# Performance work log

Measured on AMD Instinct MI355X. Metric: run time of the kernel, lower is better.

Reference implementation:

```python
import jax, jax.numpy as jnp
import numpy as np

N_NODES = 50000
N_EDGES = 1600000
NFEAT = 512
HIDDEN = 128
NUM_CLASSES = 40
DROPOUT = 0.5


def setup_inputs() -> dict:
    key = jax.random.key(0)
    ks = jax.random.split(key, 8)
    x = jax.random.normal(ks[0], (N_NODES, NFEAT), dtype=jnp.float32)
    edge_row = jax.random.randint(ks[1], (N_EDGES,), 0, N_NODES, dtype=jnp.int32)
    edge_col = jax.random.randint(ks[2], (N_EDGES,), 0, N_NODES, dtype=jnp.int32)
    edge_vals = jax.random.uniform(ks[3], (N_EDGES,), dtype=jnp.float32)
    # uniform(-stdv, stdv) init as in reset_parameters
    stdv1 = 1.0 / np.sqrt(HIDDEN)
    stdv2 = 1.0 / np.sqrt(NUM_CLASSES)
    W1 = jax.random.uniform(ks[4], (NFEAT, HIDDEN), dtype=jnp.float32, minval=-stdv1, maxval=stdv1)
    b1 = jax.random.uniform(ks[5], (HIDDEN,), dtype=jnp.float32, minval=-stdv1, maxval=stdv1)
    W2 = jax.random.uniform(ks[6], (HIDDEN, NUM_CLASSES), dtype=jnp.float32, minval=-stdv2, maxval=stdv2)
    b2 = jax.random.uniform(ks[7], (NUM_CLASSES,), dtype=jnp.float32, minval=-stdv2, maxval=stdv2)
    return {"x": x, "edge_row": edge_row, "edge_col": edge_col, "edge_vals": edge_vals,
            "W1": W1, "b1": b1, "W2": W2, "b2": b2}


def _spmm(edge_row, edge_col, edge_vals, support):
    # out[i] = sum_{e: row[e]==i} vals[e] * support[col[e]]  (sparse adj @ support)
    msgs = support[edge_col] * edge_vals[:, None]  # [E, F]
    return jax.ops.segment_sum(msgs, edge_row, num_segments=N_NODES)


def _dropout(x, rate, key):
    keep = 1.0 - rate
    mask = jax.random.bernoulli(key, keep, x.shape)
    return jnp.where(mask, x / keep, jnp.zeros((), x.dtype))


def reference(x, edge_row, edge_col, edge_vals, W1, b1, W2, b2):
    # layer 1: GCN conv + bias + relu + dropout (training=True)
    h = _spmm(edge_row, edge_col, edge_vals, x @ W1) + b1  # [N, H]
    h = jax.nn.relu(h)
    h = _dropout(h, DROPOUT, jax.random.key(42))
    # layer 2: GCN conv + bias + relu
    out = _spmm(edge_row, edge_col, edge_vals, h @ W2) + b2  # [N, C]
    return jax.nn.relu(out)
```

## Files before the change

kernel.cpp:

```cpp
#include <hip/hip_runtime.h>
#include <hip/hip_bf16.h>

#define N_NODES 50000
#define N_EDGES 1600000
#define NFEAT   512
#define HIDDEN  128
#define NCLASS  40

#define NBUCK 391
#define ROWS_PER_BUCKET 128
#define BUCK_PAD 4608

#define W1T_BLOCKS 256
#define GEMM1_BLOCKS 391
#define PART_T 4096
#define PART_BLOCKS 391

#define FUSED_LDS 37944

typedef short short8 __attribute__((ext_vector_type(8)));
typedef float f32x4  __attribute__((ext_vector_type(4)));

__device__ __forceinline__ unsigned short f2bu(float f) {
  __hip_bfloat16 h = __float2bfloat16(f);
  return *reinterpret_cast<unsigned short*>(&h);
}

__device__ __forceinline__ unsigned rotl32(unsigned x, int n) {
  return (x << n) | (x >> (32 - n));
}

__device__ __forceinline__ unsigned threefry_bits(unsigned x1) {
  unsigned x0 = 0u;
  const unsigned ks0 = 0u, ks1 = 42u, ks2 = 0x1BD11BDAu ^ 42u;
  x0 += ks0; x1 += ks1;
#define TFR(r) { x0 += x1; x1 = rotl32(x1, (r)); x1 ^= x0; }
  TFR(13) TFR(15) TFR(26) TFR(6)
  x0 += ks1; x1 += ks2 + 1u;
  TFR(17) TFR(29) TFR(16) TFR(24)
  x0 += ks2; x1 += ks0 + 2u;
  TFR(13) TFR(15) TFR(26) TFR(6)
  x0 += ks0; x1 += ks1 + 3u;
  TFR(17) TFR(29) TFR(16) TFR(24)
  x0 += ks1; x1 += ks2 + 4u;
  TFR(13) TFR(15) TFR(26) TFR(6)
  x0 += ks2; x1 += ks0 + 5u;
#undef TFR
  return x0 ^ x1;
}

__global__ __launch_bounds__(256) void init_w1t_kernel(
    const float* __restrict__ W1, unsigned short* __restrict__ W1T,
    int* __restrict__ gcur) {
  if (blockIdx.x < W1T_BLOCKS) {
    int id = blockIdx.x * 256 + threadIdx.x;
    int n = id & 127, k = id >> 7;
    W1T[n * NFEAT + k] = f2bu(W1[k * HIDDEN + n]);
  } else {
    int b = threadIdx.x;
    if (b < NBUCK) gcur[b] = b * BUCK_PAD;
    b += 256;
    if (b < NBUCK) gcur[b] = b * BUCK_PAD;
  }
}

__device__ __forceinline__ void gemm1_body(
    int bid, char* smem, const float* __restrict__ x,
    const unsigned short* __restrict__ W1T,
    unsigned short* __restrict__ support) {
  short8* As = (short8*)smem;
  short8* Bs = (short8*)(smem + 8192);
  const int t = threadIdx.x;
  const int lane = t & 63;
  const int w = t >> 6;
  const int quad = lane >> 4;
  const int l15 = lane & 15;
  const int node_base = bid * 128;
  const int mbase = (w >> 1) * 64;
  const int nbase = (w & 1) * 64;

  f32x4 acc[4][4] = {};

  for (int k0 = 0; k0 < NFEAT; k0 += 32) {
#pragma unroll
    for (int i = 0; i < 2; i++) {
      int lin = i * 256 + t;
      int n = lin >> 2, q = lin & 3;
      int row = node_base + n;
      if (row >= N_NODES) row = N_NODES - 1;
      const float* src = &x[(size_t)row * NFEAT + k0 + q * 8];
      float4 a = *(const float4*)src;
      float4 b = *(const float4*)(src + 4);
      short8 p;
      p[0] = (short)f2bu(a.x); p[1] = (short)f2bu(a.y);
      p[2] = (short)f2bu(a.z); p[3] = (short)f2bu(a.w);
      p[4] = (short)f2bu(b.x); p[5] = (short)f2bu(b.y);
      p[6] = (short)f2bu(b.z); p[7] = (short)f2bu(b.w);
      As[q * 128 + n] = p;
      Bs[q * 128 + n] = *(const short8*)&W1T[(size_t)n * NFEAT + k0 + q * 8];
    }
    __syncthreads();
    short8 af[4], bfr[4];
#pragma unroll
    for (int mt = 0; mt < 4; mt++)
      af[mt] = As[quad * 128 + mbase + mt * 16 + l15];
#pragma unroll
    for (int nt = 0; nt < 4; nt++)
      bfr[nt] = Bs[quad * 128 + nbase + nt * 16 + l15];
#pragma unroll
    for (int mt = 0; mt < 4; mt++)
#pragma unroll
      for (int nt = 0; nt < 4; nt++)
        acc[mt][nt] = __builtin_amdgcn_mfma_f32_16x16x32_bf16(
            af[mt], bfr[nt], acc[mt][nt], 0, 0, 0);
    __syncthreads();
  }

#pragma unroll
  for (int mt = 0; mt < 4; mt++)
#pragma unroll
    for (int nt = 0; nt < 4; nt++)
#pragma unroll
      for (int r = 0; r < 4; r++) {
        int row = node_base + mbase + mt * 16 + quad * 4 + r;
        int col = nbase + nt * 16 + l15;
        if (row < N_NODES)
          support[(size_t)row * HIDDEN + col] = f2bu(acc[mt][nt][r]);
      }
}

__device__ __forceinline__ void partition_body(
    int bid, char* smem, const int* __restrict__ erow,
    const int* __restrict__ ecol, const float* __restrict__ evals,
    int* __restrict__ gcur, uint2* __restrict__ eb) {
  uint2* sorted = (uint2*)smem;
  int* cnt   = (int*)(smem + 32768);
  int* shift = (int*)(smem + 32768 + 1564);
  int* ssc   = (int*)(smem + 32768 + 3128);
  const int t = threadIdx.x;
  const int base = bid * PART_T;

  if (t < NBUCK) cnt[t] = 0;
  if (t + 256 < NBUCK) cnt[t + 256] = 0;
  __syncthreads();

  uint2 er[16];
  unsigned short loc[16];
#pragma unroll
  for (int k = 0; k < 16; k++) {
    int idx = base + k * 256 + t;
    if (idx < N_EDGES) {
      int r = erow[idx];
      er[k].y = (unsigned)r;
      er[k].x = (unsigned)ecol[idx] | ((unsigned)f2bu(evals[idx]) << 16);
      loc[k] = (unsigned short)atomicAdd(&cnt[r >> 7], 1);
    } else {
      er[k].y = 0xffffffffu;
    }
  }
  __syncthreads();

  ssc[t] = (t < NBUCK) ? cnt[t] : 0;
  ssc[t + 256] = (t + 256 < NBUCK) ? cnt[t + 256] : 0;
  __syncthreads();
#pragma unroll
  for (int off = 1; off < 512; off <<= 1) {
    int v0 = (t >= off) ? ssc[t - off] : 0;
    int v1 = ssc[t + 256 - off];
    __syncthreads();
    ssc[t] += v0; ssc[t + 256] += v1;
    __syncthreads();
  }

  for (int b = t; b < NBUCK; b += 256) {
    int c = cnt[b];
    if (c > 0) {
      int lb = ssc[b] - c;
      int gb = atomicAdd(&gcur[b], c);
      shift[b] = gb - lb;
    }
  }
#pragma unroll
  for (int k = 0; k < 16; k++) {
    if (er[k].y != 0xffffffffu) {
      int b = (int)(er[k].y >> 7);
      sorted[ssc[b] - cnt[b] + (int)loc[k]] = er[k];
    }
  }
  __syncthreads();

  const int total = ssc[NBUCK - 1];
  for (int i = t; i < total; i += 256) {
    uint2 e = sorted[i];
    eb[shift[e.y >> 7] + i] = e;
  }
}

__global__ __launch_bounds__(256) void part_gemm1_kernel(
    const int* __restrict__ erow, const int* __restrict__ ecol,
    const float* __restrict__ evals, int* __restrict__ gcur,
    uint2* __restrict__ eb, const float* __restrict__ x,
    const unsigned short* __restrict__ W1T,
    unsigned short* __restrict__ support) {
  __shared__ char smem[FUSED_LDS];
  if (blockIdx.x < PART_BLOCKS)
    partition_body(blockIdx.x, smem, erow, ecol, evals, gcur, eb);
  else
    gemm1_body(blockIdx.x - PART_BLOCKS, smem, x, W1T, support);
}

__global__ __launch_bounds__(512) void csr_build_kernel(
    const uint2* __restrict__ eb, const int* __restrict__ gcur,
    unsigned* __restrict__ csr, int* __restrict__ rowptr,
    int* __restrict__ rowend) {
  __shared__ int cnt[ROWS_PER_BUCKET];
  __shared__ int sc[ROWS_PER_BUCKET];
  __shared__ int cur[ROWS_PER_BUCKET];
  const int t = threadIdx.x;
  const int b = blockIdx.x;
  if (t < ROWS_PER_BUCKET) cnt[t] = 0;
  __syncthreads();
  const int beg = b * BUCK_PAD;
  const int end = gcur[b];
  for (int j = beg + t; j < end; j += 512)
    atomicAdd(&cnt[eb[j].y & 127u], 1);
  __syncthreads();
  if (t < ROWS_PER_BUCKET) sc[t] = cnt[t];
  __syncthreads();
#pragma unroll
  for (int off = 1; off < ROWS_PER_BUCKET; off <<= 1) {
    int v = 0;
    if (t >= off && t < ROWS_PER_BUCKET) v = sc[t - off];
    __syncthreads();
    if (t < ROWS_PER_BUCKET) sc[t] += v;
    __syncthreads();
  }
  if (t < ROWS_PER_BUCKET) {
    int excl = sc[t] - cnt[t];
    cur[t] = excl;
    int row = b * ROWS_PER_BUCKET + t;
    if (row < N_NODES) {
      rowptr[row] = beg + excl;
      rowend[row] = beg + sc[t];
    }
  }
  __syncthreads();
  for (int j = beg + t; j < end; j += 512) {
    uint2 e = eb[j];
    int p = atomicAdd(&cur[e.y & 127u], 1);
    csr[beg + p] = e.x;
  }
}

__global__ __launch_bounds__(256) void spmm1_fused(
    const unsigned* __restrict__ csr, const int* __restrict__ rowptr,
    const int* __restrict__ rowend,
    const unsigned* __restrict__ sup,
    const float* __restrict__ b1, const float* __restrict__ W2,
    unsigned* __restrict__ h2u) {
  __shared__ float Ws[HIDDEN * NCLASS];
  __shared__ unsigned hrow[4][64];
  const int t = threadIdx.x;
#pragma unroll
  for (int i = 0; i < 20; i++) Ws[i * 256 + t] = W2[i * 256 + t];
  __syncthreads();

  const int row = blockIdx.x * 4 + (t >> 6);
  const int wv = t >> 6;
  const int lane = t & 63;
  const int beg = __builtin_amdgcn_readfirstlane(rowptr[row]);
  const int end = __builtin_amdgcn_readfirstlane(rowend[row]);
  float ax = 0.f, ay = 0.f;
  int j = beg;
  for (; j + 15 < end; j += 16) {
    unsigned ps[16];
#pragma unroll
    for (int k = 0; k < 16; k++)
      ps[k] = __builtin_amdgcn_readfirstlane(csr[j + k]);
    unsigned u[16];
#pragma unroll
    for (int k = 0; k < 16; k++)
      u[k] = sup[(size_t)(ps[k] & 0xffffu) * 64 + lane];
#pragma unroll
    for (int k = 0; k < 16; k++) {
      float v = __uint_as_float(ps[k] & 0xffff0000u);
      ax += v * __uint_as_float(u[k] << 16);
      ay += v * __uint_as_float(u[k] & 0xffff0000u);
    }
  }
  for (; j + 7 < end; j += 8) {
    unsigned ps[8];
#pragma unroll
    for (int k = 0; k < 8; k++)
      ps[k] = __builtin_amdgcn_readfirstlane(csr[j + k]);
    unsigned u[8];
#pragma unroll
    for (int k = 0; k < 8; k++)
      u[k] = sup[(size_t)(ps[k] & 0xffffu) * 64 + lane];
#pragma unroll
    for (int k = 0; k < 8; k++) {
      float v = __uint_as_float(ps[k] & 0xffff0000u);
      ax += v * __uint_as_float(u[k] << 16);
      ay += v * __uint_as_float(u[k] & 0xffff0000u);
    }
  }
  for (; j + 1 < end; j += 2) {
    unsigned p0 = __builtin_amdgcn_readfirstlane(csr[j]);
    unsigned p1 = __builtin_amdgcn_readfirstlane(csr[j + 1]);
    unsigned u0 = sup[(size_t)(p0 & 0xffffu) * 64 + lane];
    unsigned u1 = sup[(size_t)(p1 & 0xffffu) * 64 + lane];
    float v0 = __uint_as_float(p0 & 0xffff0000u);
    float v1 = __uint_as_float(p1 & 0xffff0000u);
    ax += v0 * __uint_as_float(u0 << 16) + v1 * __uint_as_float(u1 << 16);
    ay += v0 * __uint_as_float(u0 & 0xffff0000u) +
          v1 * __uint_as_float(u1 & 0xffff0000u);
  }
  if (j < end) {
    unsigned p0 = __builtin_amdgcn_readfirstlane(csr[j]);
    unsigned u0 = sup[(size_t)(p0 & 0xffffu) * 64 + lane];
    float v0 = __uint_as_float(p0 & 0xffff0000u);
    ax += v0 * __uint_as_float(u0 << 16);
    ay += v0 * __uint_as_float(u0 & 0xffff0000u);
  }
  const unsigned i0 = (unsigned)row * HIDDEN + lane * 2;
  float vx = fmaxf(ax + b1[lane * 2], 0.f);
  float vy = fmaxf(ay + b1[lane * 2 + 1], 0.f);
  vx = (threefry_bits(i0) >> 31) ? 0.f : 2.f * vx;
  vy = (threefry_bits(i0 + 1) >> 31) ? 0.f : 2.f * vy;
  hrow[wv][lane] = (unsigned)f2bu(vx) | ((unsigned)f2bu(vy) << 16);
  __syncthreads();

  float accv = 0.f;
  if (lane < NCLASS) {
#pragma unroll 8
    for (int i = 0; i < 64; i++) {
      unsigned u = hrow[wv][i];
      float h0 = __uint_as_float(u << 16);
      float h1 = __uint_as_float(u & 0xffff0000u);
      accv += h0 * Ws[(2 * i) * NCLASS + lane] +
              h1 * Ws[(2 * i + 1) * NCLASS + lane];
    }
    float other = __shfl_xor(accv, 1);
    if (!(lane & 1))
      h2u[(unsigned)row * 20 + (lane >> 1)] =
          (unsigned)f2bu(accv) | ((unsigned)f2bu(other) << 16);
  }
}

__global__ __launch_bounds__(256) void spmm2_fused(
    const unsigned* __restrict__ csr, const int* __restrict__ rowptr,
    const int* __restrict__ rowend,
    const unsigned* __restrict__ h2u,
    const float* __restrict__ b2, float* __restrict__ out) {
  const int row = blockIdx.x * 4 + (threadIdx.x >> 6);
  const int lane = threadIdx.x & 63;
  const int half = lane >> 5;
  const int il = lane & 31;
  const unsigned ilc = (il < 20) ? (unsigned)il : 19u;
  const int beg = rowptr[row], end = rowend[row];
  float ax = 0.f, ay = 0.f;
  int j = beg + half;
  for (; j + 6 < end; j += 8) {
    unsigned p[4], u[4];
#pragma unroll
    for (int k = 0; k < 4; k++) p[k] = csr[j + 2 * k];
#pragma unroll
    for (int k = 0; k < 4; k++) u[k] = h2u[(p[k] & 0xffffu) * 20 + ilc];
#pragma unroll
    for (int k = 0; k < 4; k++) {
      float v = __uint_as_float(p[k] & 0xffff0000u);
      ax += v * __uint_as_float(u[k] << 16);
      ay += v * __uint_as_float(u[k] & 0xffff0000u);
    }
  }
  for (; j + 2 < end; j += 4) {
    unsigned p0 = csr[j];
    unsigned p1 = csr[j + 2];
    unsigned u0 = h2u[(p0 & 0xffffu) * 20 + ilc];
    unsigned u1 = h2u[(p1 & 0xffffu) * 20 + ilc];
    float v0 = __uint_as_float(p0 & 0xffff0000u);
    float v1 = __uint_as_float(p1 & 0xffff0000u);
    ax += v0 * __uint_as_float(u0 << 16) + v1 * __uint_as_float(u1 << 16);
    ay += v0 * __uint_as_float(u0 & 0xffff0000u) +
          v1 * __uint_as_float(u1 & 0xffff0000u);
  }
  for (; j < end; j += 2) {
    unsigned p0 = csr[j];
    unsigned u0 = h2u[(p0 & 0xffffu) * 20 + ilc];
    float v0 = __uint_as_float(p0 & 0xffff0000u);
    ax += v0 * __uint_as_float(u0 << 16);
    ay += v0 * __uint_as_float(u0 & 0xffff0000u);
  }
  ax += __shfl_xor(ax, 32);
  ay += __shfl_xor(ay, 32);
  if (half == 0 && il < 20) {
    float2 r;
    r.x = fmaxf(ax + b2[il * 2], 0.f);
    r.y = fmaxf(ay + b2[il * 2 + 1], 0.f);
    *(float2*)&out[(unsigned)row * NCLASS + il * 2] = r;
  }
}

extern "C" void kernel_launch(void* const* d_in, const int* in_sizes, int n_in,
                              void* d_out, int out_size, void* d_ws,
                              size_t ws_size, hipStream_t stream) {
  const float* x     = (const float*)d_in[0];
  const int*   erow  = (const int*)d_in[1];
  const int*   ecol  = (const int*)d_in[2];
  const float* evals = (const float*)d_in[3];
  const float* W1    = (const float*)d_in[4];
  const float* b1    = (const float*)d_in[5];
  const float* W2    = (const float*)d_in[6];
  const float* b2    = (const float*)d_in[7];
  float* out = (float*)d_out;

  char* base = (char*)d_ws;
  unsigned short* support = (unsigned short*)base;
  uint2*          eb  = (uint2*)(base + 12800000);
  unsigned*       h2  = (unsigned*)(base + 27213824);
  unsigned short* W1T = (unsigned short*)(base + 31213824);
  unsigned*       csr = (unsigned*)(base + 31344896);
  int* rowptr = (int*)(base + 38551808);
  int* rowend = (int*)(base + 38751808);
  int* gcur   = (int*)(base + 38951808);

  init_w1t_kernel<<<W1T_BLOCKS + 1, 256, 0, stream>>>(W1, W1T, gcur);
  part_gemm1_kernel<<<PART_BLOCKS + GEMM1_BLOCKS, 256, 0, stream>>>(
      erow, ecol, evals, gcur, eb, x, W1T, support);
  csr_build_kernel<<<NBUCK, 512, 0, stream>>>(eb, gcur, csr, rowptr, rowend);
  spmm1_fused<<<N_NODES / 4, 256, 0, stream>>>(
      csr, rowptr, rowend, (const unsigned*)support, b1, W2, h2);
  spmm2_fused<<<N_NODES / 4, 256, 0, stream>>>(csr, rowptr, rowend,
                                               (const unsigned*)h2, b2, out);
}
```

Measured before the change: 313.3 us.

## Store support in fp32, use fp32 hidden row, and restructure partition into two-pass bucketing

The GEMM1 output (support) is now stored as fp32 rather than bf16, and spmm1 gathers float2 per lane while keeping the post-dropout hidden row in fp32 for the W2 product. The edge partition step now handles 8192 edges per block and runs two passes: it counts first, then scatters using atomic cursors, so it no longer holds edges in registers. These changes improve accuracy and alter partition occupancy, but they double the bytes gathered in spmm1 and double the LDS per block.

Result: slower. 346.5 us (+10.6%).

```diff
diff --git a/kernel.cpp b/kernel.cpp
--- a/kernel.cpp
+++ b/kernel.cpp
@@ -13,10 +13,10 @@
 
 #define W1T_BLOCKS 256
 #define GEMM1_BLOCKS 391
-#define PART_T 4096
-#define PART_BLOCKS 391
-
-#define FUSED_LDS 37944
+#define PART_T 8192
+#define PART_BLOCKS 196
+
+#define FUSED_LDS 72276
 
 typedef short short8 __attribute__((ext_vector_type(8)));
 typedef float f32x4  __attribute__((ext_vector_type(4)));
@@ -67,7 +67,7 @@
 __device__ __forceinline__ void gemm1_body(
     int bid, char* smem, const float* __restrict__ x,
     const unsigned short* __restrict__ W1T,
-    unsigned short* __restrict__ support) {
+    float* __restrict__ support) {
   short8* As = (short8*)smem;
   short8* Bs = (short8*)(smem + 8192);
   const int t = threadIdx.x;
@@ -125,7 +125,7 @@
         int row = node_base + mbase + mt * 16 + quad * 4 + r;
         int col = nbase + nt * 16 + l15;
         if (row < N_NODES)
-          support[(size_t)row * HIDDEN + col] = f2bu(acc[mt][nt][r]);
+          support[(size_t)row * HIDDEN + col] = acc[mt][nt][r];
       }
 }
 
@@ -134,9 +134,10 @@
     const int* __restrict__ ecol, const float* __restrict__ evals,
     int* __restrict__ gcur, uint2* __restrict__ eb) {
   uint2* sorted = (uint2*)smem;
-  int* cnt   = (int*)(smem + 32768);
-  int* shift = (int*)(smem + 32768 + 1564);
-  int* ssc   = (int*)(smem + 32768 + 3128);
+  int* cnt   = (int*)(smem + 65536);
+  int* cur   = (int*)(smem + 65536 + 1564);
+  int* shift = (int*)(smem + 65536 + 3128);
+  int* ssc   = (int*)(smem + 65536 + 4692);
   const int t = threadIdx.x;
   const int base = bid * PART_T;
 
@@ -144,47 +145,42 @@
   if (t + 256 < NBUCK) cnt[t + 256] = 0;
   __syncthreads();
 
-  uint2 er[16];
-  unsigned short loc[16];
-#pragma unroll
-  for (int k = 0; k < 16; k++) {
+#pragma unroll 8
+  for (int k = 0; k < 32; k++) {
+    int idx = base + k * 256 + t;
+    if (idx < N_EDGES) atomicAdd(&cnt[erow[idx] >> 7], 1);
+  }
+  __syncthreads();
+
+  ssc[t] = (t < NBUCK) ? cnt[t] : 0;
+  ssc[t + 256] = (t + 256 < NBUCK) ? cnt[t + 256] : 0;
+  __syncthreads();
+#pragma unroll
+  for (int off = 1; off < 512; off <<= 1) {
+    int v0 = (t >= off) ? ssc[t - off] : 0;
+    int v1 = ssc[t + 256 - off];
+    __syncthreads();
+    ssc[t] += v0; ssc[t + 256] += v1;
+    __syncthreads();
+  }
+
+  for (int b = t; b < NBUCK; b += 256) {
+    int c = cnt[b];
+    int lb = ssc[b] - c;
+    cur[b] = lb;
+    if (c > 0) shift[b] = atomicAdd(&gcur[b], c) - lb;
+  }
+  __syncthreads();
+
+#pragma unroll 8
+  for (int k = 0; k < 32; k++) {
     int idx = base + k * 256 + t;
     if (idx < N_EDGES) {
       int r = erow[idx];
-      er[k].y = (unsigned)r;
-      er[k].x = (unsigned)ecol[idx] | ((unsigned)f2bu(evals[idx]) << 16);
-      loc[k] = (unsigned short)atomicAdd(&cnt[r >> 7], 1);
-    } else {
-      er[k].y = 0xffffffffu;
-    }
-  }
-  __syncthreads();
-
-  ssc[t] = (t < NBUCK) ? cnt[t] : 0;
-  ssc[t + 256] = (t + 256 < NBUCK) ? cnt[t + 256] : 0;
-  __syncthreads();
-#pragma unroll
-  for (int off = 1; off < 512; off <<= 1) {
-    int v0 = (t >= off) ? ssc[t - off] : 0;
-    int v1 = ssc[t + 256 - off];
-    __syncthreads();
-    ssc[t] += v0; ssc[t + 256] += v1;
-    __syncthreads();
-  }
-
-  for (int b = t; b < NBUCK; b += 256) {
-    int c = cnt[b];
-    if (c > 0) {
-      int lb = ssc[b] - c;
-      int gb = atomicAdd(&gcur[b], c);
-      shift[b] = gb - lb;
-    }
-  }
-#pragma unroll
-  for (int k = 0; k < 16; k++) {
-    if (er[k].y != 0xffffffffu) {
-      int b = (int)(er[k].y >> 7);
-      sorted[ssc[b] - cnt[b] + (int)loc[k]] = er[k];
+      unsigned rec = (unsigned)ecol[idx] | ((unsigned)f2bu(evals[idx]) << 16);
+      int p = atomicAdd(&cur[r >> 7], 1);
+      uint2 e; e.x = rec; e.y = (unsigned)r;
+      sorted[p] = e;
     }
   }
   __syncthreads();
@@ -201,7 +197,7 @@
     const float* __restrict__ evals, int* __restrict__ gcur,
     uint2* __restrict__ eb, const float* __restrict__ x,
     const unsigned short* __restrict__ W1T,
-    unsigned short* __restrict__ support) {
+    float* __restrict__ support) {
   __shared__ char smem[FUSED_LDS];
   if (blockIdx.x < PART_BLOCKS)
     partition_body(blockIdx.x, smem, erow, ecol, evals, gcur, eb);
@@ -255,11 +251,11 @@
 __global__ __launch_bounds__(256) void spmm1_fused(
     const unsigned* __restrict__ csr, const int* __restrict__ rowptr,
     const int* __restrict__ rowend,
-    const unsigned* __restrict__ sup,
+    const float2* __restrict__ sup,
     const float* __restrict__ b1, const float* __restrict__ W2,
     unsigned* __restrict__ h2u) {
   __shared__ float Ws[HIDDEN * NCLASS];
-  __shared__ unsigned hrow[4][64];
+  __shared__ float hrowf[4][HIDDEN];
   const int t = threadIdx.x;
 #pragma unroll
   for (int i = 0; i < 20; i++) Ws[i * 256 + t] = W2[i * 256 + t];
@@ -277,15 +273,15 @@
 #pragma unroll
     for (int k = 0; k < 16; k++)
       ps[k] = __builtin_amdgcn_readfirstlane(csr[j + k]);
-    unsigned u[16];
+    float2 u[16];
 #pragma unroll
     for (int k = 0; k < 16; k++)
       u[k] = sup[(size_t)(ps[k] & 0xffffu) * 64 + lane];
 #pragma unroll
     for (int k = 0; k < 16; k++) {
       float v = __uint_as_float(ps[k] & 0xffff0000u);
-      ax += v * __uint_as_float(u[k] << 16);
-      ay += v * __uint_as_float(u[k] & 0xffff0000u);
+      ax += v * u[k].x;
+      ay += v * u[k].y;
     }
   }
   for (; j + 7 < end; j += 8) {
@@ -293,53 +289,48 @@
 #pragma unroll
     for (int k = 0; k < 8; k++)
       ps[k] = __builtin_amdgcn_readfirstlane(csr[j + k]);
-    unsigned u[8];
+    float2 u[8];
 #pragma unroll
     for (int k = 0; k < 8; k++)
       u[k] = sup[(size_t)(ps[k] & 0xffffu) * 64 + lane];
 #pragma unroll
     for (int k = 0; k < 8; k++) {
       float v = __uint_as_float(ps[k] & 0xffff0000u);
-      ax += v * __uint_as_float(u[k] << 16);
-      ay += v * __uint_as_float(u[k] & 0xffff0000u);
+      ax += v * u[k].x;
+      ay += v * u[k].y;
     }
   }
   for (; j + 1 < end; j += 2) {
     unsigned p0 = __builtin_amdgcn_readfirstlane(csr[j]);
     unsigned p1 = __builtin_amdgcn_readfirstlane(csr[j + 1]);
-    unsigned u0 = sup[(size_t)(p0 & 0xffffu) * 64 + lane];
-    unsigned u1 = sup[(size_t)(p1 & 0xffffu) * 64 + lane];
+    float2 u0 = sup[(size_t)(p0 & 0xffffu) * 64 + lane];
+    float2 u1 = sup[(size_t)(p1 & 0xffffu) * 64 + lane];
     float v0 = __uint_as_float(p0 & 0xffff0000u);
     float v1 = __uint_as_float(p1 & 0xffff0000u);
-    ax += v0 * __uint_as_float(u0 << 16) + v1 * __uint_as_float(u1 << 16);
-    ay += v0 * __uint_as_float(u0 & 0xffff0000u) +
-          v1 * __uint_as_float(u1 & 0xffff0000u);
+    ax += v0 * u0.x + v1 * u1.x;
+    ay += v0 * u0.y + v1 * u1.y;
   }
   if (j < end) {
     unsigned p0 = __builtin_amdgcn_readfirstlane(csr[j]);
-    unsigned u0 = sup[(size_t)(p0 & 0xffffu) * 64 + lane];
+    float2 u0 = sup[(size_t)(p0 & 0xffffu) * 64 + lane];
     float v0 = __uint_as_float(p0 & 0xffff0000u);
-    ax += v0 * __uint_as_float(u0 << 16);
-    ay += v0 * __uint_as_float(u0 & 0xffff0000u);
+    ax += v0 * u0.x;
+    ay += v0 * u0.y;
   }
   const unsigned i0 = (unsigned)row * HIDDEN + lane * 2;
   float vx = fmaxf(ax + b1[lane * 2], 0.f);
   float vy = fmaxf(ay + b1[lane * 2 + 1], 0.f);
   vx = (threefry_bits(i0) >> 31) ? 0.f : 2.f * vx;
   vy = (threefry_bits(i0 + 1) >> 31) ? 0.f : 2.f * vy;
-  hrow[wv][lane] = (unsigned)f2bu(vx) | ((unsigned)f2bu(vy) << 16);
+  hrowf[wv][lane * 2] = vx;
+  hrowf[wv][lane * 2 + 1] = vy;
   __syncthreads();
 
   float accv = 0.f;
   if (lane < NCLASS) {
-#pragma unroll 8
-    for (int i = 0; i < 64; i++) {
-      unsigned u = hrow[wv][i];
-      float h0 = __uint_as_float(u << 16);
-      float h1 = __uint_as_float(u & 0xffff0000u);
-      accv += h0 * Ws[(2 * i) * NCLASS + lane] +
-              h1 * Ws[(2 * i + 1) * NCLASS + lane];
-    }
+#pragma unroll
+    for (int i = 0; i < HIDDEN; i++)
+      accv += hrowf[wv][i] * Ws[i * NCLASS + lane];
     float other = __shfl_xor(accv, 1);
     if (!(lane & 1))
       h2u[(unsigned)row * 20 + (lane >> 1)] =
@@ -415,21 +406,21 @@
   float* out = (float*)d_out;
 
   char* base = (char*)d_ws;
-  unsigned short* support = (unsigned short*)base;
-  uint2*          eb  = (uint2*)(base + 12800000);
-  unsigned*       h2  = (unsigned*)(base + 27213824);
-  unsigned short* W1T = (unsigned short*)(base + 31213824);
-  unsigned*       csr = (unsigned*)(base + 31344896);
-  int* rowptr = (int*)(base + 38551808);
-  int* rowend = (int*)(base + 38751808);
-  int* gcur   = (int*)(base + 38951808);
+  float*          support = (float*)base;
+  uint2*          eb  = (uint2*)(base + 25600000);
+  unsigned*       h2  = (unsigned*)(base + 40013824);
+  unsigned short* W1T = (unsigned short*)(base + 44013824);
+  unsigned*       csr = (unsigned*)(base + 44144896);
+  int* rowptr = (int*)(base + 51351808);
+  int* rowend = (int*)(base + 51551808);
+  int* gcur   = (int*)(base + 51751808);
 
   init_w1t_kernel<<<W1T_BLOCKS + 1, 256, 0, stream>>>(W1, W1T, gcur);
   part_gemm1_kernel<<<PART_BLOCKS + GEMM1_BLOCKS, 256, 0, stream>>>(
       erow, ecol, evals, gcur, eb, x, W1T, support);
   csr_build_kernel<<<NBUCK, 512, 0, stream>>>(eb, gcur, csr, rowptr, rowend);
   spmm1_fused<<<N_NODES / 4, 256, 0, stream>>>(
-      csr, rowptr, rowend, (const unsigned*)support, b1, W2, h2);
+      csr, rowptr, rowend, (const float2*)support, b1, W2, h2);
   spmm2_fused<<<N_NODES / 4, 256, 0, stream>>>(csr, rowptr, rowend,
                                                (const unsigned*)h2, b2, out);
 }
```
